# Performance work log

Measured on AMD Instinct MI355X. Metric: run time of the kernel, lower is better.

## Reference

```python
import jax, jax.numpy as jnp
import numpy as np

B, S, H = 1, 4096, 2048
NH, HD = 16, 128  # num_heads, head_dim = H // NH


def setup_inputs() -> dict:
    key = jax.random.key(0)
    k1, k2, k3 = jax.random.split(key, 3)
    x = jax.random.normal(k1, (B, S, H), dtype=jnp.float32)
    w_qkv = jax.random.normal(k2, (3 * H, H), dtype=jnp.float32) * (1.0 / np.sqrt(H))
    w_out = jax.random.normal(k3, (H, H), dtype=jnp.float32) * (1.0 / np.sqrt(H))
    return {"x": x, "w_qkv": w_qkv, "w_out": w_out}


def reference(x, w_qkv, w_out):
    b, s, _ = x.shape
    # qkv projection: torch Linear computes x @ W^T
    qkv = jnp.einsum('bsh,oh->bso', x, w_qkv)
    qkv = qkv.reshape(b, s, 3, NH, HD).transpose(2, 0, 3, 1, 4)  # [3,B,NH,S,HD]
    q, k, v = qkv[0], qkv[1], qkv[2]
    # world_size == 1 -> single ring step == full attention with online softmax
    scores = jnp.einsum('bhqd,bhkd->bhqk', q, k) / np.sqrt(HD)
    m = jnp.max(scores, axis=-1, keepdims=True)          # running max (single step)
    p = jnp.exp(scores - m)                              # scores_exp
    out = jnp.einsum('bhqk,bhkd->bhqd', p, v)
    denom = jnp.sum(p, axis=-1, keepdims=True) + 1e-8    # running_sum + eps
    out = out / denom
    out = out.transpose(0, 2, 1, 3).reshape(b, s, H)     # [B,S,H]
    return jnp.einsum('bsh,oh->bso', out, w_out)
```

## Files before the change

kernel.cpp:

```cpp
#include <hip/hip_runtime.h>
#include <stdint.h>

typedef __attribute__((ext_vector_type(4))) float f32x4;
typedef __attribute__((ext_vector_type(16))) float f32x16;
typedef __attribute__((ext_vector_type(8))) short bf16x8;
typedef unsigned short u16;

#define MFMA(a, b, c) __builtin_amdgcn_mfma_f32_16x16x32_bf16(a, b, c, 0, 0, 0)
#define MFMA32(a, b, c) __builtin_amdgcn_mfma_f32_32x32x16_bf16(a, b, c, 0, 0, 0)
#define EXP2(x) __builtin_amdgcn_exp2f(x)

__device__ __forceinline__ u16 f2bf(float f) {
  union { float f; unsigned u; } x; x.f = f;
  unsigned r = x.u + 0x7fffu + ((x.u >> 16) & 1u);
  return (u16)(r >> 16);
}

__device__ __forceinline__ unsigned cvtpk(float lo, float hi) {
  unsigned r;
  asm("v_cvt_pk_bf16_f32 %0, %1, %2" : "=v"(r) : "v"(lo), "v"(hi));
  return r;
}

__device__ __forceinline__ void pl32swap(unsigned& a, unsigned& b) {
  asm volatile("v_permlane32_swap_b32 %0, %1" : "+v"(a), "+v"(b));
}

__device__ __forceinline__ void gload16(const void* g, void* l) {
  __builtin_amdgcn_global_load_lds(
      (const __attribute__((address_space(1))) unsigned int*)g,
      (__attribute__((address_space(3))) unsigned int*)l, 16, 0, 0);
}

__global__ void __launch_bounds__(256) cast_bf16(const float* __restrict__ in,
                                                 u16* __restrict__ out, int n4) {
  int i = blockIdx.x * 256 + threadIdx.x;
  if (i >= n4) return;
  float4 v = reinterpret_cast<const float4*>(in)[i];
  ushort4 o;
  o.x = f2bf(v.x); o.y = f2bf(v.y); o.z = f2bf(v.z); o.w = f2bf(v.w);
  reinterpret_cast<ushort4*>(out)[i] = o;
}

template <int EPI>
__global__ void __launch_bounds__(256, 2)
gemm_bt(const u16* __restrict__ A, const u16* __restrict__ B,
        void* __restrict__ C0, void* __restrict__ C1, void* __restrict__ C2,
        int M, int N, int K, int MB) {
  __shared__ alignas(16) u16 sm[8192];
  const int tid = threadIdx.x;
  const int w = tid >> 6, lane = tid & 63;
  const int lr = lane & 15, g = lane >> 4;
  const int gb = (blockIdx.x & 7) * ((int)gridDim.x >> 3) + (blockIdx.x >> 3);
  const int mb = gb % MB, nb = gb / MB;
  const int m0 = mb * 128, n0 = nb * 128;

  const u16* src[4];
  u16* dst[4];
#pragma unroll
  for (int i = 0; i < 4; ++i) {
    int c = w * 4 + i;
    int r = (c & 7) * 16 + (lane >> 2);
    int sb = (lane & 3) ^ ((r >> 1) & 3);
    src[i] = (c < 8) ? (A + (size_t)(m0 + r) * K + sb * 8)
                     : (B + (size_t)(n0 + r) * K + sb * 8);
    dst[i] = &sm[c * 512];
  }

  f32x4 acc[4][4];
#pragma unroll
  for (int x = 0; x < 4; ++x)
#pragma unroll
    for (int y = 0; y < 4; ++y) acc[x][y] = f32x4{0.f, 0.f, 0.f, 0.f};

  const int rowb = (w >> 1) * 64, colb = (w & 1) * 64;
  const int nk = K >> 5;
  for (int kt = 0; kt < nk; ++kt) {
#pragma unroll
    for (int i = 0; i < 4; ++i) gload16(src[i] + kt * 32, dst[i]);
    __syncthreads();
    bf16x8 af[4], bfr[4];
#pragma unroll
    for (int mi = 0; mi < 4; ++mi) {
      int r = rowb + mi * 16 + lr;
      af[mi] = *(const bf16x8*)((const char*)sm + r * 64 +
                                ((g * 16) ^ (((r >> 1) & 3) << 4)));
    }
#pragma unroll
    for (int ni = 0; ni < 4; ++ni) {
      int r = colb + ni * 16 + lr;
      bfr[ni] = *(const bf16x8*)((const char*)sm + 8192 + r * 64 +
                                 ((g * 16) ^ (((r >> 1) & 3) << 4)));
    }
#pragma unroll
    for (int mi = 0; mi < 4; ++mi)
#pragma unroll
      for (int ni = 0; ni < 4; ++ni)
        acc[mi][ni] = MFMA(af[mi], bfr[ni], acc[mi][ni]);
    __syncthreads();
  }

  if (EPI == 0) {
    const float qs = 0.08838834764831845f * 1.4426950408889634f;
    u16* qo = (u16*)C0;
    u16* ko = (u16*)C1;
    u16* vo = (u16*)C2;
#pragma unroll
    for (int mi = 0; mi < 4; ++mi) {
      int s0 = m0 + rowb + mi * 16 + g * 4;
#pragma unroll
      for (int ni = 0; ni < 4; ++ni) {
        int n = n0 + colb + ni * 16 + lr;
        int t = n >> 11, hh = (n >> 7) & 15, d = n & 127;
        if (t == 2) {
          ushort4 pk;
          pk.x = f2bf(acc[mi][ni][0]);
          pk.y = f2bf(acc[mi][ni][1]);
          pk.z = f2bf(acc[mi][ni][2]);
          pk.w = f2bf(acc[mi][ni][3]);
          *(ushort4*)(vo + (size_t)(hh * 128 + d) * 4096 + s0) = pk;
        } else {
          float sc = (t == 0) ? qs : 1.f;
          u16* dq = (t == 0 ? qo : ko) + (size_t)(hh * 4096 + s0) * 128 + d;
#pragma unroll
          for (int j = 0; j < 4; ++j) dq[(size_t)j * 128] = f2bf(acc[mi][ni][j] * sc);
        }
      }
    }
  } else {
    float* C = (float*)C0;
#pragma unroll
    for (int mi = 0; mi < 4; ++mi)
#pragma unroll
      for (int ni = 0; ni < 4; ++ni) {
        size_t r0 = (size_t)(m0 + rowb + mi * 16 + g * 4);
        int cn = n0 + colb + ni * 16 + lr;
#pragma unroll
        for (int j = 0; j < 4; ++j) C[(r0 + j) * N + cn] = acc[mi][ni][j];
      }
  }
}

__global__ void __launch_bounds__(256, 2)
attn_kernel(const u16* __restrict__ qg, const u16* __restrict__ kg,
            const u16* __restrict__ vtg, u16* __restrict__ og) {
  __shared__ alignas(16) u16 sm[32768];
  const int tid = threadIdx.x;
  const int w = tid >> 6, lane = tid & 63;
  const int ql = lane & 31, hl = lane >> 5;
  const int gb = (blockIdx.x & 7) * 64 + (blockIdx.x >> 3);
  const int h = gb >> 5;
  const int qb = gb & 31;

  const u16* ssrc[8];
  u16* sdst[8];
  size_t sstep;
  if (w < 2) {
    sstep = 64 * 128;
#pragma unroll
    for (int i = 0; i < 8; ++i) {
      int c = (w & 1) * 8 + i;
      int r = c * 4 + (lane >> 4);
      int sb = (lane & 15) ^ (r & 15);
      ssrc[i] = kg + (size_t)(h * 4096 + r) * 128 + sb * 8;
      sdst[i] = &sm[c * 512];
    }
  } else {
    sstep = 64;
#pragma unroll
    for (int i = 0; i < 8; ++i) {
      int c = (w & 1) * 8 + i;
      int j = c * 4 + (lane >> 4);
      int x = (lane & 15) ^ (j & 15);
      int e = x >> 3, b = x & 7;
      ssrc[i] = vtg + (size_t)(h * 128 + 2 * j + e) * 4096 + b * 8;
      sdst[i] = &sm[16384 + c * 512];
    }
  }

  const u16* qrow = qg + (size_t)(h * 4096 + qb * 128 + w * 32 + ql) * 128 + hl * 8;
  bf16x8 qf[8];
#pragma unroll
  for (int s = 0; s < 8; ++s) qf[s] = *(const bf16x8*)(qrow + s * 16);

  f32x16 of[4];
#pragma unroll
  for (int i = 0; i < 4; ++i)
#pragma unroll
    for (int r = 0; r < 16; ++r) of[i][r] = 0.f;
  float mrun = -1e30f, lsum = 0.f;
  const float thr = 6.0f;

#pragma unroll
  for (int i = 0; i < 8; ++i) gload16(ssrc[i], sdst[i]);

  const int kxor = (ql & 15) << 4;
  const int ve8 = (ql & 1) << 3, vxor = ql >> 1;
  for (int t = 0; t < 64; ++t) {
    const int cur = t & 1;
    asm volatile("s_waitcnt vmcnt(0)" ::: "memory");
    __builtin_amdgcn_s_barrier();
    asm volatile("" ::: "memory");
    if (t + 1 < 64) {
      const int nb = (t + 1) & 1;
#pragma unroll
      for (int i = 0; i < 8; ++i)
        gload16(ssrc[i] + (size_t)(t + 1) * sstep, sdst[i] + nb * 8192);
    }
    const char* kbuf = (const char*)sm + cur * 16384;
    const char* vbuf = (const char*)sm + 32768 + cur * 16384;

    f32x16 st0, st1;
#pragma unroll
    for (int r = 0; r < 16; ++r) { st0[r] = 0.f; st1[r] = 0.f; }
    __builtin_amdgcn_s_setprio(1);
#pragma unroll
    for (int s = 0; s < 8; ++s) {
      int off = ((s * 2 + hl) << 4) ^ kxor;
      bf16x8 k0 = *(const bf16x8*)(kbuf + ql * 256 + off);
      bf16x8 k1 = *(const bf16x8*)(kbuf + (32 + ql) * 256 + off);
      st0 = MFMA32(k0, qf[s], st0);
      st1 = MFMA32(k1, qf[s], st1);
    }
    __builtin_amdgcn_s_setprio(0);

    float tmax = -1e30f;
#pragma unroll
    for (int r = 0; r < 16; ++r) tmax = fmaxf(tmax, fmaxf(st0[r], st1[r]));
    tmax = fmaxf(tmax, __shfl_xor(tmax, 32));
    if (!__all(tmax - mrun <= thr)) {
      float mnew = fmaxf(mrun, tmax);
      float esc = EXP2(mrun - mnew);
#pragma unroll
      for (int db = 0; db < 4; ++db)
#pragma unroll
        for (int r = 0; r < 16; ++r) of[db][r] *= esc;
      lsum *= esc;
      mrun = mnew;
    }
    float psum = 0.f;
    unsigned pk0[8], pk1[8];
#pragma unroll
    for (int i = 0; i < 8; ++i) {
      float a0 = EXP2(st0[2 * i] - mrun);
      float b0 = EXP2(st0[2 * i + 1] - mrun);
      float a1 = EXP2(st1[2 * i] - mrun);
      float b1 = EXP2(st1[2 * i + 1] - mrun);
      psum += (a0 + b0) + (a1 + b1);
      pk0[i] = cvtpk(a0, b0);
      pk1[i] = cvtpk(a1, b1);
    }
    psum += __shfl_xor(psum, 32);
    lsum += psum;

    pl32swap(pk0[0], pk0[2]); pl32swap(pk0[1], pk0[3]);
    pl32swap(pk0[4], pk0[6]); pl32swap(pk0[5], pk0[7]);
    pl32swap(pk1[0], pk1[2]); pl32swap(pk1[1], pk1[3]);
    pl32swap(pk1[4], pk1[6]); pl32swap(pk1[5], pk1[7]);
    union U { unsigned u[4]; bf16x8 v; };
    U paf[4];
#pragma unroll
    for (int i = 0; i < 4; ++i) { paf[0].u[i] = pk0[i]; paf[1].u[i] = pk0[4 + i]; }
#pragma unroll
    for (int i = 0; i < 4; ++i) { paf[2].u[i] = pk1[i]; paf[3].u[i] = pk1[4 + i]; }

    __builtin_amdgcn_s_setprio(1);
#pragma unroll
    for (int db = 0; db < 4; ++db) {
      const char* vrow = vbuf + (db * 16 + vxor) * 256;
#pragma unroll
      for (int kp = 0; kp < 4; ++kp) {
        int m = (ve8 | (kp * 2 + hl)) ^ vxor;
        bf16x8 vf = *(const bf16x8*)(vrow + m * 16);
        of[db] = MFMA32(vf, paf[kp].v, of[db]);
      }
    }
    __builtin_amdgcn_s_setprio(0);
    asm volatile("" ::: "memory");
  }

  float linv = 1.f / (lsum + 1e-8f);
  size_t qrow_o = (size_t)(qb * 128 + w * 32 + ql) * 2048 + h * 128;
#pragma unroll
  for (int db = 0; db < 4; ++db)
#pragma unroll
    for (int u = 0; u < 4; ++u) {
      ushort4 pk;
      pk.x = f2bf(of[db][4 * u + 0] * linv);
      pk.y = f2bf(of[db][4 * u + 1] * linv);
      pk.z = f2bf(of[db][4 * u + 2] * linv);
      pk.w = f2bf(of[db][4 * u + 3] * linv);
      *(ushort4*)(og + qrow_o + db * 32 + 8 * u + hl * 4) = pk;
    }
}

extern "C" void kernel_launch(void* const* d_in, const int* in_sizes, int n_in,
                              void* d_out, int out_size, void* d_ws, size_t ws_size,
                              hipStream_t stream) {
  const float* x = (const float*)d_in[0];
  const float* w_qkv = (const float*)d_in[1];
  const float* w_out = (const float*)d_in[2];

  char* ws = (char*)d_ws;
  u16* xb = (u16*)(ws + 0);
  u16* wqkvb = (u16*)(ws + 16777216);
  u16* woutb = (u16*)(ws + 41943040);
  u16* qb = (u16*)(ws + 50331648);
  u16* kb = (u16*)(ws + 67108864);
  u16* vtb = (u16*)(ws + 83886080);
  u16* aob = (u16*)(ws + 100663296);

  cast_bf16<<<8192, 256, 0, stream>>>(x, xb, 2097152);
  cast_bf16<<<12288, 256, 0, stream>>>(w_qkv, wqkvb, 3145728);
  cast_bf16<<<4096, 256, 0, stream>>>(w_out, woutb, 1048576);

  gemm_bt<0><<<32 * 48, 256, 0, stream>>>(xb, wqkvb, qb, kb, vtb, 4096, 6144, 2048, 32);
  attn_kernel<<<512, 256, 0, stream>>>(qb, kb, vtb, aob);
  gemm_bt<1><<<32 * 16, 256, 0, stream>>>(aob, woutb, d_out, nullptr, nullptr, 4096, 2048, 2048, 32);
}
```

Before: 356.8 us.

## Add 256x256-tile 8-wave GEMM with staged prefetch for QKV projection

```diff
diff --git a/kernel.cpp b/kernel.cpp
--- a/kernel.cpp
+++ b/kernel.cpp
@@ -9,6 +9,8 @@
 #define MFMA(a, b, c) __builtin_amdgcn_mfma_f32_16x16x32_bf16(a, b, c, 0, 0, 0)
 #define MFMA32(a, b, c) __builtin_amdgcn_mfma_f32_32x32x16_bf16(a, b, c, 0, 0, 0)
 #define EXP2(x) __builtin_amdgcn_exp2f(x)
+#define FENCE asm volatile("" ::: "memory")
+#define BARRIER do { FENCE; __builtin_amdgcn_s_barrier(); FENCE; } while (0)
 
 __device__ __forceinline__ u16 f2bf(float f) {
   union { float f; unsigned u; } x; x.f = f;
@@ -40,6 +42,177 @@
   ushort4 o;
   o.x = f2bf(v.x); o.y = f2bf(v.y); o.z = f2bf(v.z); o.w = f2bf(v.w);
   reinterpret_cast<ushort4*>(out)[i] = o;
+}
+
+template <int EPI>
+__global__ void __launch_bounds__(512)
+gemm8(const u16* __restrict__ A, const u16* __restrict__ B,
+      void* __restrict__ C0, void* __restrict__ C1, void* __restrict__ C2,
+      int M, int N, int K, int MBt) {
+  __shared__ alignas(16) char smb[131072];
+  const int tid = threadIdx.x;
+  const int w = tid >> 6, lane = tid & 63;
+  const int lr = lane & 15, g = lane >> 4;
+  const int wm = w >> 2, wn = w & 3;
+  const int gb = (blockIdx.x & 7) * ((int)gridDim.x >> 3) + (blockIdx.x >> 3);
+  const int mb = gb % MBt, nb = gb / MBt;
+  const int m0 = mb * 256, n0 = nb * 256;
+  const int NT = K >> 6, NIT = NT >> 1;
+
+  const int l8 = lane >> 3, l7 = lane & 7;
+  const int csb = (l7 ^ l8) * 16;
+  const char* asrcb[2];
+  const char* bsrcb[2];
+  unsigned adst[2], bdst[2];
+#pragma unroll
+  for (int j = 0; j < 2; ++j) {
+    int c = 2 * w + j;
+    int ra = (c & 7) * 8 + ((c >> 3) << 7) + l8;
+    asrcb[j] = (const char*)(A + (size_t)(m0 + ra) * K) + csb;
+    adst[j] = (unsigned)(ra * 128 + l7 * 16);
+    int rb = (c & 3) * 8 + ((c >> 2) << 6) + l8;
+    bsrcb[j] = (const char*)(B + (size_t)(n0 + rb) * K) + csb;
+    bdst[j] = (unsigned)(rb * 128 + l7 * 16);
+  }
+  const size_t arow64 = (size_t)64 * K * 2;
+  const size_t brow32 = (size_t)32 * K * 2;
+
+#define STG(kt, u)                                                            \
+  do {                                                                        \
+    if ((kt) < NT) {                                                          \
+      int _d = ((kt) & 1) ? 32768 : 0;                                        \
+      size_t _ko = (size_t)(kt) * 128;                                        \
+      if ((u) == 0) {                                                         \
+        gload16(asrcb[0] + _ko, smb + _d + adst[0]);                          \
+        gload16(asrcb[1] + _ko, smb + _d + adst[1]);                          \
+      } else if ((u) == 1) {                                                  \
+        gload16(bsrcb[0] + _ko, smb + 65536 + _d + bdst[0]);                  \
+        gload16(bsrcb[1] + _ko, smb + 65536 + _d + bdst[1]);                  \
+      } else if ((u) == 2) {                                                  \
+        gload16(asrcb[0] + arow64 + _ko, smb + _d + 8192 + adst[0]);          \
+        gload16(asrcb[1] + arow64 + _ko, smb + _d + 8192 + adst[1]);          \
+      } else {                                                                \
+        gload16(bsrcb[0] + brow32 + _ko, smb + 65536 + _d + 4096 + bdst[0]);  \
+        gload16(bsrcb[1] + brow32 + _ko, smb + 65536 + _d + 4096 + bdst[1]);  \
+      }                                                                       \
+    }                                                                         \
+  } while (0)
+
+  f32x4 acc[8][4];
+#pragma unroll
+  for (int x = 0; x < 8; ++x)
+#pragma unroll
+    for (int y = 0; y < 4; ++y) acc[x][y] = f32x4{0.f, 0.f, 0.f, 0.f};
+  bf16x8 af[4][2], bf01[2][2], bf23[2][2];
+  const int aoff0 = ((g) ^ (lr & 7)) << 4;
+  const int aoff1 = ((4 + g) ^ (lr & 7)) << 4;
+  const int arow = (wm * 128 + lr) * 128;
+  const int brow = (wn * 64 + lr) * 128;
+
+  auto LDA = [&](const char* base, int mih) {
+#pragma unroll
+    for (int mi = 0; mi < 4; ++mi) {
+      const char* p = base + arow + (mih * 64 + mi * 16) * 128;
+      af[mi][0] = *(const bf16x8*)(p + aoff0);
+      af[mi][1] = *(const bf16x8*)(p + aoff1);
+    }
+  };
+  auto LDB = [&](const char* base, bf16x8 (*bfr)[2], int nih) {
+#pragma unroll
+    for (int ni = 0; ni < 2; ++ni) {
+      const char* p = base + brow + (nih * 32 + ni * 16) * 128;
+      bfr[ni][0] = *(const bf16x8*)(p + aoff0);
+      bfr[ni][1] = *(const bf16x8*)(p + aoff1);
+    }
+  };
+  auto MM = [&](int mih, int nih, bf16x8 (*bfr)[2]) {
+    __builtin_amdgcn_s_setprio(1);
+#pragma unroll
+    for (int mi = 0; mi < 4; ++mi)
+#pragma unroll
+      for (int ni = 0; ni < 2; ++ni) {
+        acc[mih * 4 + mi][nih * 2 + ni] =
+            MFMA(af[mi][0], bfr[ni][0], acc[mih * 4 + mi][nih * 2 + ni]);
+        acc[mih * 4 + mi][nih * 2 + ni] =
+            MFMA(af[mi][1], bfr[ni][1], acc[mih * 4 + mi][nih * 2 + ni]);
+      }
+    __builtin_amdgcn_s_setprio(0);
+  };
+
+  STG(0, 0); STG(0, 1); STG(0, 2); STG(0, 3);
+  STG(1, 0); STG(1, 1); STG(1, 2);
+  asm volatile("s_waitcnt vmcnt(6)" ::: "memory");
+  BARRIER;
+
+  const char* A0 = smb;
+  const char* B0 = smb + 65536;
+  const char* A1 = smb + 32768;
+  const char* B1 = smb + 65536 + 32768;
+
+  for (int it = 0; it < NIT; ++it) {
+    const int t0 = 2 * it;
+    const bool lastit = (it == NIT - 1);
+    LDA(A0, 0); LDB(B0, bf01, 0); STG(t0 + 1, 3);
+    BARRIER; MM(0, 0, bf01); BARRIER;
+    LDB(B0, bf23, 1); STG(t0 + 2, 0);
+    BARRIER; MM(0, 1, bf23); BARRIER;
+    LDA(A0, 1); STG(t0 + 2, 1);
+    BARRIER; MM(1, 1, bf23); BARRIER;
+    STG(t0 + 2, 2);
+    if (lastit) asm volatile("s_waitcnt vmcnt(0)" ::: "memory");
+    else        asm volatile("s_waitcnt vmcnt(6)" ::: "memory");
+    BARRIER; MM(1, 0, bf01); BARRIER;
+    LDA(A1, 0); LDB(B1, bf01, 0); STG(t0 + 2, 3);
+    BARRIER; MM(0, 0, bf01); BARRIER;
+    LDB(B1, bf23, 1); STG(t0 + 3, 0);
+    BARRIER; MM(0, 1, bf23); BARRIER;
+    LDA(A1, 1); STG(t0 + 3, 1);
+    BARRIER; MM(1, 1, bf23); BARRIER;
+    STG(t0 + 3, 2);
+    asm volatile("s_waitcnt vmcnt(6)" ::: "memory");
+    BARRIER; MM(1, 0, bf01); BARRIER;
+  }
+#undef STG
+
+  if (EPI == 0) {
+    const float qs = 0.08838834764831845f * 1.4426950408889634f;
+    u16* qo = (u16*)C0;
+    u16* ko = (u16*)C1;
+    u16* vo = (u16*)C2;
+#pragma unroll
+    for (int mi = 0; mi < 8; ++mi) {
+      int s0 = m0 + wm * 128 + mi * 16 + g * 4;
+#pragma unroll
+      for (int ni = 0; ni < 4; ++ni) {
+        int n = n0 + wn * 64 + ni * 16 + lr;
+        int t = n >> 11, hh = (n >> 7) & 15, d = n & 127;
+        if (t == 2) {
+          ushort4 pk;
+          pk.x = f2bf(acc[mi][ni][0]);
+          pk.y = f2bf(acc[mi][ni][1]);
+          pk.z = f2bf(acc[mi][ni][2]);
+          pk.w = f2bf(acc[mi][ni][3]);
+          *(ushort4*)(vo + (size_t)(hh * 128 + d) * 4096 + s0) = pk;
+        } else {
+          float sc = (t == 0) ? qs : 1.f;
+          u16* dq = (t == 0 ? qo : ko) + (size_t)(hh * 4096 + s0) * 128 + d;
+#pragma unroll
+          for (int j = 0; j < 4; ++j) dq[(size_t)j * 128] = f2bf(acc[mi][ni][j] * sc);
+        }
+      }
+    }
+  } else {
+    float* C = (float*)C0;
+#pragma unroll
+    for (int mi = 0; mi < 8; ++mi)
+#pragma unroll
+      for (int ni = 0; ni < 4; ++ni) {
+        size_t r0 = (size_t)(m0 + wm * 128 + mi * 16 + g * 4);
+        int cn = n0 + wn * 64 + ni * 16 + lr;
+#pragma unroll
+        for (int j = 0; j < 4; ++j) C[(r0 + j) * N + cn] = acc[mi][ni][j];
+      }
+  }
 }
 
 template <int EPI>
@@ -100,45 +273,16 @@
     __syncthreads();
   }
 
-  if (EPI == 0) {
-    const float qs = 0.08838834764831845f * 1.4426950408889634f;
-    u16* qo = (u16*)C0;
-    u16* ko = (u16*)C1;
-    u16* vo = (u16*)C2;
-#pragma unroll
-    for (int mi = 0; mi < 4; ++mi) {
-      int s0 = m0 + rowb + mi * 16 + g * 4;
-#pragma unroll
-      for (int ni = 0; ni < 4; ++ni) {
-        int n = n0 + colb + ni * 16 + lr;
-        int t = n >> 11, hh = (n >> 7) & 15, d = n & 127;
-        if (t == 2) {
-          ushort4 pk;
-          pk.x = f2bf(acc[mi][ni][0]);
-          pk.y = f2bf(acc[mi][ni][1]);
-          pk.z = f2bf(acc[mi][ni][2]);
-          pk.w = f2bf(acc[mi][ni][3]);
-          *(ushort4*)(vo + (size_t)(hh * 128 + d) * 4096 + s0) = pk;
-        } else {
-          float sc = (t == 0) ? qs : 1.f;
-          u16* dq = (t == 0 ? qo : ko) + (size_t)(hh * 4096 + s0) * 128 + d;
-#pragma unroll
-          for (int j = 0; j < 4; ++j) dq[(size_t)j * 128] = f2bf(acc[mi][ni][j] * sc);
-        }
-      }
-    }
-  } else {
-    float* C = (float*)C0;
-#pragma unroll
-    for (int mi = 0; mi < 4; ++mi)
-#pragma unroll
-      for (int ni = 0; ni < 4; ++ni) {
-        size_t r0 = (size_t)(m0 + rowb + mi * 16 + g * 4);
-        int cn = n0 + colb + ni * 16 + lr;
-#pragma unroll
-        for (int j = 0; j < 4; ++j) C[(r0 + j) * N + cn] = acc[mi][ni][j];
-      }
-  }
+  float* C = (float*)C0;
+#pragma unroll
+  for (int mi = 0; mi < 4; ++mi)
+#pragma unroll
+    for (int ni = 0; ni < 4; ++ni) {
+      size_t r0 = (size_t)(m0 + rowb + mi * 16 + g * 4);
+      int cn = n0 + colb + ni * 16 + lr;
+#pragma unroll
+      for (int j = 0; j < 4; ++j) C[(r0 + j) * N + cn] = acc[mi][ni][j];
+    }
 }
 
 __global__ void __launch_bounds__(256, 2)
@@ -200,7 +344,7 @@
     const int cur = t & 1;
     asm volatile("s_waitcnt vmcnt(0)" ::: "memory");
     __builtin_amdgcn_s_barrier();
-    asm volatile("" ::: "memory");
+    FENCE;
     if (t + 1 < 64) {
       const int nb = (t + 1) & 1;
 #pragma unroll
@@ -276,7 +420,7 @@
       }
     }
     __builtin_amdgcn_s_setprio(0);
-    asm volatile("" ::: "memory");
+    FENCE;
   }
 
   float linv = 1.f / (lsum + 1e-8f);
@@ -314,7 +458,7 @@
   cast_bf16<<<12288, 256, 0, stream>>>(w_qkv, wqkvb, 3145728);
   cast_bf16<<<4096, 256, 0, stream>>>(w_out, woutb, 1048576);
 
-  gemm_bt<0><<<32 * 48, 256, 0, stream>>>(xb, wqkvb, qb, kb, vtb, 4096, 6144, 2048, 32);
+  gemm8<0><<<384, 512, 0, stream>>>(xb, wqkvb, qb, kb, vtb, 4096, 6144, 2048, 16);
   attn_kernel<<<512, 256, 0, stream>>>(qb, kb, vtb, aob);
   gemm_bt<1><<<32 * 16, 256, 0, stream>>>(aob, woutb, d_out, nullptr, nullptr, 4096, 2048, 2048, 32);
 }
```

Result: no change. 350.2 us (-1.9%).
